# Performance work log

Hardware: AMD Instinct MI355X
Metric: run time of the kernel (lower is better)

## Reference

```python
import jax, jax.numpy as jnp
import numpy as np

DIM = 1024
HEADS = 16
HEAD_DIM = DIM // HEADS
SCALE = HEAD_DIM ** -0.5


def setup_inputs() -> dict:
    key = jax.random.key(0)
    k_x, k_wqkv, k_bqkv, k_wp, k_bp = jax.random.split(key, 5)
    B, N, C = 8, 1024, DIM
    lim_qkv = 1.0 / np.sqrt(C)
    x = jax.random.normal(k_x, (B, N, C), dtype=jnp.float32)
    # store weights in [in, out] layout (torch Linear weight is [out,in]; y = x @ W.T + b)
    W_qkv = jax.random.uniform(k_wqkv, (C, 3 * C), dtype=jnp.float32, minval=-lim_qkv, maxval=lim_qkv)
    b_qkv = jax.random.uniform(k_bqkv, (3 * C,), dtype=jnp.float32, minval=-lim_qkv, maxval=lim_qkv)
    W_proj = jax.random.uniform(k_wp, (C, C), dtype=jnp.float32, minval=-lim_qkv, maxval=lim_qkv)
    b_proj = jax.random.uniform(k_bp, (C,), dtype=jnp.float32, minval=-lim_qkv, maxval=lim_qkv)
    return {"x": x, "W_qkv": W_qkv, "b_qkv": b_qkv, "W_proj": W_proj, "b_proj": b_proj}


def reference(x, W_qkv, b_qkv, W_proj, b_proj):
    B, N, C = x.shape
    H, D = HEADS, C // HEADS
    qkv = x @ W_qkv + b_qkv                          # [B, N, 3C]
    qkv = qkv.reshape(B, N, 3, H, D)
    q, k, v = jnp.moveaxis(qkv, 2, 0)                # each [B, N, H, D]
    q = q.transpose(0, 2, 1, 3)                      # [B, H, N, D]
    k = k.transpose(0, 2, 1, 3)
    v = v.transpose(0, 2, 1, 3)
    attn = jnp.einsum("bhnd,bhmd->bhnm", q, k) * SCALE
    attn = jax.nn.softmax(attn, axis=-1)
    out = jnp.einsum("bhnm,bhmd->bhnd", attn, v)     # [B, H, N, D]
    out = out.transpose(0, 2, 1, 3).reshape(B, N, C)
    return out @ W_proj + b_proj
```

## Files before the change

### kernel.cpp

```cpp
#include <hip/hip_runtime.h>
#include <hip/hip_bf16.h>


using bf16x8 = __attribute__((ext_vector_type(8))) short;
using f32x4  = __attribute__((ext_vector_type(4))) float;
using u16    = unsigned short;
using u16x4  = __attribute__((ext_vector_type(4))) unsigned short;
using u16x8  = __attribute__((ext_vector_type(8))) unsigned short;
using u32x2  = __attribute__((ext_vector_type(2))) unsigned int;

__device__ __forceinline__ u16 f2bf(float f) {
  unsigned int u = __float_as_uint(f);
  u += 0x7FFFu + ((u >> 16) & 1u);
  return (u16)(u >> 16);
}
__device__ __forceinline__ float bf2f(u16 h) {
  return __uint_as_float(((unsigned int)h) << 16);
}
__device__ __forceinline__ unsigned cvt_pk_bf16(float a, float b) {
  unsigned r;
  asm("v_cvt_pk_bf16_f32 %0, %1, %2" : "=v"(r) : "v"(a), "v"(b));
  return r;
}
__device__ __forceinline__ float fexp2(float x) {
#if __has_builtin(__builtin_amdgcn_exp2f)
  return __builtin_amdgcn_exp2f(x);
#else
  return exp2f(x);
#endif
}

__device__ __forceinline__ void gload16(const u16* g, u16* lbase, int lane) {
#if __has_builtin(__builtin_amdgcn_global_load_lds)
  __builtin_amdgcn_global_load_lds(
      (const __attribute__((address_space(1))) void*)g,
      (__attribute__((address_space(3))) void*)lbase, 16, 0, 0);
#else
  *(u16x8*)(lbase + (size_t)lane * 8) = *(const u16x8*)g;
#endif
}

__global__ __launch_bounds__(256) void convert_f32_bf16(
    const float* __restrict__ in, u16* __restrict__ out)
{
  size_t i = ((size_t)blockIdx.x * 256 + threadIdx.x) * 8;
  f32x4 a = *(const f32x4*)(in + i);
  f32x4 b = *(const f32x4*)(in + i + 4);
  u16x8 h = { f2bf(a.x), f2bf(a.y), f2bf(a.z), f2bf(a.w),
              f2bf(b.x), f2bf(b.y), f2bf(b.z), f2bf(b.w) };
  *(u16x8*)(out + i) = h;
}

__global__ __launch_bounds__(256) void transpose_w(
    const float* __restrict__ W, u16* __restrict__ Wt, int K, int N)
{
  __shared__ float T[64][65];
  const int t = threadIdx.x;
  const int n0 = blockIdx.x * 64, k0 = blockIdx.y * 64;
  const int r = t >> 4, c4 = (t & 15) * 4;
  #pragma unroll
  for (int i = 0; i < 4; ++i) {
    f32x4 v = *(const f32x4*)&W[(size_t)(k0 + r + i * 16) * N + n0 + c4];
    T[r + i * 16][c4 + 0] = v.x;
    T[r + i * 16][c4 + 1] = v.y;
    T[r + i * 16][c4 + 2] = v.z;
    T[r + i * 16][c4 + 3] = v.w;
  }
  __syncthreads();
  const int nr = t >> 2, cs = (t & 3) * 16;
  u16x8 h0, h1;
  #pragma unroll
  for (int j = 0; j < 8; ++j) h0[j] = f2bf(T[cs + j][nr]);
  #pragma unroll
  for (int j = 0; j < 8; ++j) h1[j] = f2bf(T[cs + 8 + j][nr]);
  u16* dst = Wt + (size_t)(n0 + nr) * K + k0 + cs;
  *(u16x8*)dst = h0;
  *(u16x8*)(dst + 8) = h1;
}

__global__ __launch_bounds__(256) void v_transpose(
    const u16* __restrict__ Vr, u16* __restrict__ Vt)
{
  __shared__ u16 T[64 * 70];
  const int bh = blockIdx.x >> 4, nc = blockIdx.x & 15;
  const int t = threadIdx.x;
  const int r = t >> 2, c = (t & 3) * 16;
  const u16* src = Vr + ((size_t)bh * 1024 + nc * 64 + r) * 64 + c;
  *(u16x8*)&T[r * 70 + c]     = *(const u16x8*)src;
  *(u16x8*)&T[r * 70 + c + 8] = *(const u16x8*)(src + 8);
  __syncthreads();
  const int d = t >> 2, n0 = (t & 3) * 16;
  u16x8 o0, o1;
  #pragma unroll
  for (int j = 0; j < 8; ++j) o0[j] = T[(n0 + j) * 70 + d];
  #pragma unroll
  for (int j = 0; j < 8; ++j) o1[j] = T[(n0 + 8 + j) * 70 + d];
  u16* dst = Vt + ((size_t)bh * 64 + d) * 1024 + nc * 64 + n0;
  *(u16x8*)dst = o0;
  *(u16x8*)(dst + 8) = o1;
}

__global__ __launch_bounds__(256, 2) void qkv_gemm2(
    const u16* __restrict__ Xb, const u16* __restrict__ Wt,
    const float* __restrict__ bias,
    u16* __restrict__ Qb, u16* __restrict__ Kb, u16* __restrict__ Vr)
{
  constexpr int KD = 1024;
  __shared__ __align__(16) u16 As[128 * 32];
  __shared__ __align__(16) u16 Bs[128 * 32];

  const int tid = threadIdx.x;
  const int lane = tid & 63, wid = tid >> 6;
  const int wr = wid >> 1, wc = wid & 1;
  const int lg = lane >> 4, lc = lane & 15;
  const int row0 = blockIdx.x * 128, col0 = blockIdx.y * 128;

  f32x4 acc[4][4];
  #pragma unroll
  for (int m = 0; m < 4; ++m)
    #pragma unroll
    for (int n = 0; n < 4; ++n) acc[m][n] = (f32x4){0.f, 0.f, 0.f, 0.f};

  const int l4 = lane >> 2, ls = (lane & 3) * 8;
  const u16* gA0 = Xb + (size_t)(row0 + wid * 16 + l4) * KD + ls;
  const u16* gB0 = Wt + (size_t)(col0 + wid * 16 + l4) * KD + ls;
  u16* lA0 = As + wid * 512;
  u16* lB0 = Bs + wid * 512;

  for (int k0 = 0; k0 < KD; k0 += 32) {
    gload16(gA0 + k0, lA0, lane);
    gload16(gA0 + 64 * KD + k0, lA0 + 2048, lane);
    gload16(gB0 + k0, lB0, lane);
    gload16(gB0 + 64 * KD + k0, lB0 + 2048, lane);
    __syncthreads();

    bf16x8 a[4], b[4];
    #pragma unroll
    for (int m = 0; m < 4; ++m)
      a[m] = *(const bf16x8*)(As + (wr * 64 + m * 16 + lc) * 32 + lg * 8);
    #pragma unroll
    for (int n = 0; n < 4; ++n)
      b[n] = *(const bf16x8*)(Bs + (wc * 64 + n * 16 + lc) * 32 + lg * 8);
    #pragma unroll
    for (int m = 0; m < 4; ++m)
      #pragma unroll
      for (int n = 0; n < 4; ++n)
        acc[m][n] = __builtin_amdgcn_mfma_f32_16x16x32_bf16(a[m], b[n], acc[m][n], 0, 0, 0);
    __syncthreads();
  }

  #pragma unroll
  for (int m = 0; m < 4; ++m) {
    #pragma unroll
    for (int n = 0; n < 4; ++n) {
      const int gcb = col0 + wc * 64 + n * 16;
      const int which = gcb >> 10;
      const int gc = gcb + lc;
      const float bv = bias[gc];
      const int ci = gc & 1023, h = ci >> 6, d = ci & 63;
      const int gr0 = row0 + wr * 64 + m * 16 + lg * 4;
      const int bb = gr0 >> 10, nn0 = gr0 & 1023;
      u16* dst = (which == 0) ? Qb : (which == 1) ? Kb : Vr;
      #pragma unroll
      for (int r = 0; r < 4; ++r)
        dst[((size_t)(bb * 16 + h) * 1024 + nn0 + r) * 64 + d] =
            f2bf(acc[m][n][r] + bv);
    }
  }
}

__global__ __launch_bounds__(256, 2) void attn_kernel(
    const u16* __restrict__ Q, const u16* __restrict__ K,
    const u16* __restrict__ Vt, u16* __restrict__ O)
{
  __shared__ __align__(16) u16 Ks[64 * 64];
  __shared__ __align__(16) u16 Vs[64 * 64];
  __shared__ __align__(16) u16 Pl[4 * 32 * 72];

  const int tid = threadIdx.x, lane = tid & 63, wid = tid >> 6;
  const int lg = lane >> 4, lc = lane & 15;
  const int bh = blockIdx.x;
  const int qt = blockIdx.y;
  const size_t base = (size_t)bh * 65536;
  const u16* Qp = Q + base;
  const u16* Kp = K + base;
  const u16* Vp = Vt + base;

  const float QSCALE = 0.125f * 1.44269504f;
  bf16x8 qf[2][2];
  #pragma unroll
  for (int f = 0; f < 2; ++f) {
    const u16* qsrc = Qp + (size_t)(qt * 128 + wid * 32 + f * 16 + lc) * 64 + lg * 8;
    #pragma unroll
    for (int ks = 0; ks < 2; ++ks) {
      u16x8 raw = *(const u16x8*)(qsrc + ks * 32);
      bf16x8 t;
      #pragma unroll
      for (int j = 0; j < 8; ++j) t[j] = (short)f2bf(bf2f(raw[j]) * QSCALE);
      qf[f][ks] = t;
    }
  }

  f32x4 o[2][4];
  #pragma unroll
  for (int f = 0; f < 2; ++f)
    #pragma unroll
    for (int d = 0; d < 4; ++d) o[f][d] = (f32x4){0.f, 0.f, 0.f, 0.f};
  float m_r[2] = {-1e30f, -1e30f};
  float l_r[2] = {0.f, 0.f};

  const int srow  = lane >> 3;
  const int sslot = (lane & 7) ^ srow;
  const u16* gK0 = Kp + (size_t)(wid * 16 + srow) * 64 + sslot * 8;
  const u16* gV0 = Vp + (size_t)(wid * 16 + srow) * 1024 + sslot * 8;
  u16* lK0 = Ks + wid * 1024;
  u16* lV0 = Vs + wid * 1024;

  const int xr = lc & 7;
  const int cof0 = ((0 + lg) ^ xr) * 8;
  const int cof1 = ((4 + lg) ^ xr) * 8;
  const int prow = (wid * 32 + lc) * 72;

  for (int kt = 0; kt < 16; ++kt) {
    gload16(gK0 + kt * 4096, lK0, lane);
    gload16(gK0 + kt * 4096 + 512, lK0 + 512, lane);
    gload16(gV0 + kt * 64, lV0, lane);
    gload16(gV0 + 8192 + kt * 64, lV0 + 512, lane);
    __syncthreads();

    f32x4 s[2][4];
    #pragma unroll
    for (int f = 0; f < 2; ++f)
      #pragma unroll
      for (int kb = 0; kb < 4; ++kb) s[f][kb] = (f32x4){0.f, 0.f, 0.f, 0.f};
    #pragma unroll
    for (int ks = 0; ks < 2; ++ks) {
      const int co = ks ? cof1 : cof0;
      #pragma unroll
      for (int kb = 0; kb < 4; ++kb) {
        bf16x8 kfr = *(const bf16x8*)(Ks + (kb * 16 + lc) * 64 + co);
        s[0][kb] = __builtin_amdgcn_mfma_f32_16x16x32_bf16(kfr, qf[0][ks], s[0][kb], 0, 0, 0);
        s[1][kb] = __builtin_amdgcn_mfma_f32_16x16x32_bf16(kfr, qf[1][ks], s[1][kb], 0, 0, 0);
      }
    }

    #pragma unroll
    for (int f = 0; f < 2; ++f) {
      f32x4 t01, t23;
      #pragma unroll
      for (int c = 0; c < 4; ++c) {
        t01[c] = fmaxf(s[f][0][c], s[f][1][c]);
        t23[c] = fmaxf(s[f][2][c], s[f][3][c]);
      }
      float t = fmaxf(fmaxf(fmaxf(t01[0], t01[1]), fmaxf(t01[2], t01[3])),
                      fmaxf(fmaxf(t23[0], t23[1]), fmaxf(t23[2], t23[3])));
      t = fmaxf(t, __shfl_xor(t, 16));
      t = fmaxf(t, __shfl_xor(t, 32));

      if (!__all((t - m_r[f]) <= 11.5f)) {
        float nm = fmaxf(m_r[f], t);
        float sc = fexp2(m_r[f] - nm);
        m_r[f] = nm;
        l_r[f] *= sc;
        #pragma unroll
        for (int r = 0; r < 4; ++r) {
          float scr = __shfl(sc, lg * 4 + r, 16);
          #pragma unroll
          for (int d = 0; d < 4; ++d) o[f][d][r] *= scr;
        }
      }

      float lsum = 0.f;
      #pragma unroll
      for (int kb = 0; kb < 4; ++kb) {
        f32x4 p;
        #pragma unroll
        for (int c = 0; c < 4; ++c) {
          p[c] = fexp2(s[f][kb][c] - m_r[f]);
          lsum += p[c];
        }
        u32x2 w = { cvt_pk_bf16(p[0], p[1]), cvt_pk_bf16(p[2], p[3]) };
        *(u32x2*)(Pl + prow + f * 1152 + kb * 16 + lg * 4) = w;
      }
      l_r[f] += lsum;
    }

    bf16x8 pa[2][2];
    #pragma unroll
    for (int f = 0; f < 2; ++f)
      #pragma unroll
      for (int ks = 0; ks < 2; ++ks)
        pa[f][ks] = *(const bf16x8*)(Pl + prow + f * 1152 + ks * 32 + lg * 8);
    #pragma unroll
    for (int d = 0; d < 4; ++d) {
      #pragma unroll
      for (int ks = 0; ks < 2; ++ks) {
        const int co = ks ? cof1 : cof0;
        bf16x8 vfr = *(const bf16x8*)(Vs + (d * 16 + lc) * 64 + co);
        o[0][d] = __builtin_amdgcn_mfma_f32_16x16x32_bf16(pa[0][ks], vfr, o[0][d], 0, 0, 0);
        o[1][d] = __builtin_amdgcn_mfma_f32_16x16x32_bf16(pa[1][ks], vfr, o[1][d], 0, 0, 0);
      }
    }
    __syncthreads();
  }

  const int b = bh >> 4, h = bh & 15;
  #pragma unroll
  for (int f = 0; f < 2; ++f) {
    float t = l_r[f];
    t += __shfl_xor(t, 16);
    t += __shfl_xor(t, 32);
    float linv = 1.0f / t;
    #pragma unroll
    for (int r = 0; r < 4; ++r) {
      float li = __shfl(linv, lg * 4 + r, 16);
      int n = qt * 128 + wid * 32 + f * 16 + lg * 4 + r;
      u16* dst = O + ((size_t)b * 1024 + n) * 1024 + h * 64 + lc;
      #pragma unroll
      for (int d = 0; d < 4; ++d) dst[d * 16] = f2bf(o[f][d][r] * li);
    }
  }
}

__global__ __launch_bounds__(256, 2) void proj_gemm2(
    const u16* __restrict__ Ab, const u16* __restrict__ Wt,
    const float* __restrict__ bias, float* __restrict__ Out)
{
  constexpr int KD = 1024, NCOL = 1024;
  __shared__ __align__(16) u16 As[128 * 32];
  __shared__ __align__(16) u16 Bs[128 * 32];

  const int tid = threadIdx.x;
  const int lane = tid & 63, wid = tid >> 6;
  const int wr = wid >> 1, wc = wid & 1;
  const int lg = lane >> 4, lc = lane & 15;
  const int row0 = blockIdx.x * 128, col0 = blockIdx.y * 128;

  f32x4 acc[4][4];
  #pragma unroll
  for (int m = 0; m < 4; ++m)
    #pragma unroll
    for (int n = 0; n < 4; ++n) acc[m][n] = (f32x4){0.f, 0.f, 0.f, 0.f};

  const int l4 = lane >> 2, ls = (lane & 3) * 8;
  const u16* gA0 = Ab + (size_t)(row0 + wid * 16 + l4) * KD + ls;
  const u16* gB0 = Wt + (size_t)(col0 + wid * 16 + l4) * KD + ls;
  u16* lA0 = As + wid * 512;
  u16* lB0 = Bs + wid * 512;

  for (int k0 = 0; k0 < KD; k0 += 32) {
    gload16(gA0 + k0, lA0, lane);
    gload16(gA0 + 64 * KD + k0, lA0 + 2048, lane);
    gload16(gB0 + k0, lB0, lane);
    gload16(gB0 + 64 * KD + k0, lB0 + 2048, lane);
    __syncthreads();

    bf16x8 a[4], b[4];
    #pragma unroll
    for (int m = 0; m < 4; ++m)
      a[m] = *(const bf16x8*)(As + (wr * 64 + m * 16 + lc) * 32 + lg * 8);
    #pragma unroll
    for (int n = 0; n < 4; ++n)
      b[n] = *(const bf16x8*)(Bs + (wc * 64 + n * 16 + lc) * 32 + lg * 8);
    #pragma unroll
    for (int m = 0; m < 4; ++m)
      #pragma unroll
      for (int n = 0; n < 4; ++n)
        acc[m][n] = __builtin_amdgcn_mfma_f32_16x16x32_bf16(a[m], b[n], acc[m][n], 0, 0, 0);
    __syncthreads();
  }

  #pragma unroll
  for (int m = 0; m < 4; ++m) {
    #pragma unroll
    for (int n = 0; n < 4; ++n) {
      #pragma unroll
      for (int r = 0; r < 4; ++r) {
        int gr = row0 + wr * 64 + m * 16 + lg * 4 + r;
        int gc = col0 + wc * 64 + n * 16 + lc;
        Out[(size_t)gr * NCOL + gc] = acc[m][n][r] + bias[gc];
      }
    }
  }
}

extern "C" void kernel_launch(void* const* d_in, const int* in_sizes, int n_in,
                              void* d_out, int out_size, void* d_ws, size_t ws_size,
                              hipStream_t stream) {
  const float* x     = (const float*)d_in[0];
  const float* W_qkv = (const float*)d_in[1];
  const float* b_qkv = (const float*)d_in[2];
  const float* W_prj = (const float*)d_in[3];
  const float* b_prj = (const float*)d_in[4];
  float* out = (float*)d_out;

  const size_t SEG = (size_t)8192 * 1024;
  char* ws = (char*)d_ws;
  u16* Xb  = (u16*)ws;
  u16* Ab  = Xb;
  u16* VtG = (u16*)(ws + SEG * 2);
  u16* Wqt = (u16*)(ws + SEG * 4);
  u16* Wpt = Wqt + (size_t)3072 * 1024;
  u16* Vr  = (u16*)(ws + 41943040);
  u16* Qb  = (u16*)d_out;
  u16* Kb  = Qb + SEG;

  convert_f32_bf16<<<4096, 256, 0, stream>>>(x, Xb);
  transpose_w<<<dim3(48, 16), 256, 0, stream>>>(W_qkv, Wqt, 1024, 3072);
  transpose_w<<<dim3(16, 16), 256, 0, stream>>>(W_prj, Wpt, 1024, 1024);
  qkv_gemm2<<<dim3(64, 24), 256, 0, stream>>>(Xb, Wqt, b_qkv, Qb, Kb, Vr);
  v_transpose<<<2048, 256, 0, stream>>>(Vr, VtG);
  attn_kernel<<<dim3(128, 8), 256, 0, stream>>>(Qb, Kb, VtG, Ab);
  proj_gemm2<<<dim3(64, 8), 256, 0, stream>>>(Ab, Wpt, b_prj, out);
}
```

Measured before the change: 167.1 us.

## Rewrite QKV and proj GEMMs with double-buffered 128x256 tiles and swizzled LDS

Replaces the two 128x128 GEMM kernels with a shared 512-thread main loop that computes 128x256 tiles and uses K-steps of 64. Global-to-LDS loads are double-buffered with explicit vmcnt waits and raw barriers, so the next stage loads while MFMAs run on the current one. An XOR swizzle on the LDS layout is meant to avoid bank conflicts, and s_setprio raises priority around the MFMA bursts. The cost is more LDS per block (96KB), one block per CU, and fewer blocks in the grid, which can reduce latency hiding.

```diff
diff --git a/kernel.cpp b/kernel.cpp
--- a/kernel.cpp
+++ b/kernel.cpp
@@ -100,71 +100,116 @@
   *(u16x8*)(dst + 8) = o1;
 }
 
-__global__ __launch_bounds__(256, 2) void qkv_gemm2(
+#define GEMM_MAIN_LOOP(ABASE, BBASE)                                          \
+  const int tid = threadIdx.x;                                                \
+  const int lane = tid & 63, wid = tid >> 6;                                  \
+  const int wr = wid >> 2, wc = wid & 3;                                      \
+  const int lg = lane >> 4, lc = lane & 15;                                   \
+  const int row0 = blockIdx.x * 128, col0 = blockIdx.y * 256;                 \
+  f32x4 acc[4][4];                                                            \
+  _Pragma("unroll")                                                           \
+  for (int m = 0; m < 4; ++m)                                                 \
+    _Pragma("unroll")                                                         \
+    for (int n = 0; n < 4; ++n) acc[m][n] = (f32x4){0.f, 0.f, 0.f, 0.f};      \
+     \
+  const int swz = ((tid & 7) ^ ((tid >> 3) & 7)) * 8;                         \
+  const u16* gA0 = (ABASE) + (size_t)(row0 + (tid >> 3)) * 1024 + swz;        \
+  const u16* gA1 = (ABASE) + (size_t)(row0 + 64 + (tid >> 3)) * 1024 + swz;   \
+  const u16* gB0 = (BBASE) + (size_t)(col0 + (tid >> 3)) * 1024 + swz;        \
+  const u16* gB1 = (BBASE) + (size_t)(col0 + 64 + (tid >> 3)) * 1024 + swz;   \
+  const u16* gB2 = (BBASE) + (size_t)(col0 + 128 + (tid >> 3)) * 1024 + swz;  \
+  const u16* gB3 = (BBASE) + (size_t)(col0 + 192 + (tid >> 3)) * 1024 + swz;  \
+  u16* lA = LA + wid * 512;                                                   \
+  u16* lB = LB + wid * 512;                                                   \
+  auto STAGE = [&](int tt) {                                                  \
+    const int bA = (tt & 1) * 8192, bB = (tt & 1) * 16384, ko = tt * 64;      \
+    gload16(gA0 + ko, lA + bA, lane);                                         \
+    gload16(gA1 + ko, lA + bA + 4096, lane);                                  \
+    gload16(gB0 + ko, lB + bB, lane);                                         \
+    gload16(gB1 + ko, lB + bB + 4096, lane);                                  \
+    gload16(gB2 + ko, lB + bB + 8192, lane);                                  \
+    gload16(gB3 + ko, lB + bB + 12288, lane);                                 \
+  };                                                                          \
+  STAGE(0);                                                                   \
+  STAGE(1);                                                                   \
+                               \
+  const int xr = lc & 7;                                                      \
+  const int sl0 = (lg ^ xr) * 8, sl1 = ((4 + lg) ^ xr) * 8;                   \
+  const int arow = (wr * 64 + lc) * 64, brow = (wc * 64 + lc) * 64;           \
+  for (int t = 0; t < 16; ++t) {                                              \
+    if (t < 15) asm volatile("s_waitcnt vmcnt(6)" ::: "memory");              \
+    else        asm volatile("s_waitcnt vmcnt(0)" ::: "memory");              \
+    __builtin_amdgcn_s_barrier();                                             \
+    const int bA = (t & 1) * 8192, bB = (t & 1) * 16384;                      \
+    _Pragma("unroll")                                                         \
+    for (int ks = 0; ks < 2; ++ks) {                                          \
+      const int sl = ks ? sl1 : sl0;                                          \
+      bf16x8 a[4], b[4];                                                      \
+      _Pragma("unroll")                                                       \
+      for (int m = 0; m < 4; ++m)                                             \
+        a[m] = *(const bf16x8*)(LA + bA + arow + m * 1024 + sl);              \
+      _Pragma("unroll")                                                       \
+      for (int n = 0; n < 4; ++n)                                             \
+        b[n] = *(const bf16x8*)(LB + bB + brow + n * 1024 + sl);              \
+      __builtin_amdgcn_s_setprio(1);                                          \
+      _Pragma("unroll")                                                       \
+      for (int m = 0; m < 4; ++m)                                             \
+        _Pragma("unroll")                                                     \
+        for (int n = 0; n < 4; ++n)                                           \
+          acc[m][n] = __builtin_amdgcn_mfma_f32_16x16x32_bf16(                \
+              a[m], b[n], acc[m][n], 0, 0, 0);                                \
+      __builtin_amdgcn_s_setprio(0);                                          \
+    }                                                                         \
+    __builtin_amdgcn_s_barrier();                                             \
+    if (t + 2 < 16) STAGE(t + 2);                                             \
+  }
+
+__global__ __launch_bounds__(512, 1) void qkv_gemm3(
     const u16* __restrict__ Xb, const u16* __restrict__ Wt,
     const float* __restrict__ bias,
     u16* __restrict__ Qb, u16* __restrict__ Kb, u16* __restrict__ Vr)
 {
-  constexpr int KD = 1024;
-  __shared__ __align__(16) u16 As[128 * 32];
-  __shared__ __align__(16) u16 Bs[128 * 32];
-
-  const int tid = threadIdx.x;
-  const int lane = tid & 63, wid = tid >> 6;
-  const int wr = wid >> 1, wc = wid & 1;
-  const int lg = lane >> 4, lc = lane & 15;
-  const int row0 = blockIdx.x * 128, col0 = blockIdx.y * 128;
-
-  f32x4 acc[4][4];
-  #pragma unroll
-  for (int m = 0; m < 4; ++m)
-    #pragma unroll
-    for (int n = 0; n < 4; ++n) acc[m][n] = (f32x4){0.f, 0.f, 0.f, 0.f};
-
-  const int l4 = lane >> 2, ls = (lane & 3) * 8;
-  const u16* gA0 = Xb + (size_t)(row0 + wid * 16 + l4) * KD + ls;
-  const u16* gB0 = Wt + (size_t)(col0 + wid * 16 + l4) * KD + ls;
-  u16* lA0 = As + wid * 512;
-  u16* lB0 = Bs + wid * 512;
-
-  for (int k0 = 0; k0 < KD; k0 += 32) {
-    gload16(gA0 + k0, lA0, lane);
-    gload16(gA0 + 64 * KD + k0, lA0 + 2048, lane);
-    gload16(gB0 + k0, lB0, lane);
-    gload16(gB0 + 64 * KD + k0, lB0 + 2048, lane);
-    __syncthreads();
-
-    bf16x8 a[4], b[4];
-    #pragma unroll
-    for (int m = 0; m < 4; ++m)
-      a[m] = *(const bf16x8*)(As + (wr * 64 + m * 16 + lc) * 32 + lg * 8);
-    #pragma unroll
-    for (int n = 0; n < 4; ++n)
-      b[n] = *(const bf16x8*)(Bs + (wc * 64 + n * 16 + lc) * 32 + lg * 8);
-    #pragma unroll
-    for (int m = 0; m < 4; ++m)
-      #pragma unroll
-      for (int n = 0; n < 4; ++n)
-        acc[m][n] = __builtin_amdgcn_mfma_f32_16x16x32_bf16(a[m], b[n], acc[m][n], 0, 0, 0);
-    __syncthreads();
-  }
-
+  __shared__ __align__(16) u16 LA[2 * 128 * 64];
+  __shared__ __align__(16) u16 LB[2 * 256 * 64];
+  GEMM_MAIN_LOOP(Xb, Wt)
+
+  const int which = col0 >> 10;
+  u16* dst = (which == 0) ? Qb : (which == 1) ? Kb : Vr;
+  const int bb = row0 >> 10, nnb = (row0 & 1023) + wr * 64;
+  const int hb = ((col0 & 1023) >> 6) + wc;
   #pragma unroll
   for (int m = 0; m < 4; ++m) {
     #pragma unroll
     for (int n = 0; n < 4; ++n) {
-      const int gcb = col0 + wc * 64 + n * 16;
-      const int which = gcb >> 10;
-      const int gc = gcb + lc;
+      const int d = n * 16 + lc;
+      const float bv = bias[col0 + wc * 64 + n * 16 + lc];
+      const int nn0 = nnb + m * 16 + lg * 4;
+      #pragma unroll
+      for (int r = 0; r < 4; ++r)
+        dst[((size_t)(bb * 16 + hb) * 1024 + nn0 + r) * 64 + d] =
+            f2bf(acc[m][n][r] + bv);
+    }
+  }
+}
+
+__global__ __launch_bounds__(512, 1) void proj_gemm3(
+    const u16* __restrict__ Ab, const u16* __restrict__ Wt,
+    const float* __restrict__ bias, float* __restrict__ Out)
+{
+  __shared__ __align__(16) u16 LA[2 * 128 * 64];
+  __shared__ __align__(16) u16 LB[2 * 256 * 64];
+  GEMM_MAIN_LOOP(Ab, Wt)
+
+  #pragma unroll
+  for (int m = 0; m < 4; ++m) {
+    #pragma unroll
+    for (int n = 0; n < 4; ++n) {
+      const int gc = col0 + wc * 64 + n * 16 + lc;
       const float bv = bias[gc];
-      const int ci = gc & 1023, h = ci >> 6, d = ci & 63;
       const int gr0 = row0 + wr * 64 + m * 16 + lg * 4;
-      const int bb = gr0 >> 10, nn0 = gr0 & 1023;
-      u16* dst = (which == 0) ? Qb : (which == 1) ? Kb : Vr;
       #pragma unroll
       for (int r = 0; r < 4; ++r)
-        dst[((size_t)(bb * 16 + h) * 1024 + nn0 + r) * 64 + d] =
-            f2bf(acc[m][n][r] + bv);
+        Out[(size_t)(gr0 + r) * 1024 + gc] = acc[m][n][r] + bv;
     }
   }
 }
@@ -322,68 +367,6 @@
   }
 }
 
-__global__ __launch_bounds__(256, 2) void proj_gemm2(
-    const u16* __restrict__ Ab, const u16* __restrict__ Wt,
-    const float* __restrict__ bias, float* __restrict__ Out)
-{
-  constexpr int KD = 1024, NCOL = 1024;
-  __shared__ __align__(16) u16 As[128 * 32];
-  __shared__ __align__(16) u16 Bs[128 * 32];
-
-  const int tid = threadIdx.x;
-  const int lane = tid & 63, wid = tid >> 6;
-  const int wr = wid >> 1, wc = wid & 1;
-  const int lg = lane >> 4, lc = lane & 15;
-  const int row0 = blockIdx.x * 128, col0 = blockIdx.y * 128;
-
-  f32x4 acc[4][4];
-  #pragma unroll
-  for (int m = 0; m < 4; ++m)
-    #pragma unroll
-    for (int n = 0; n < 4; ++n) acc[m][n] = (f32x4){0.f, 0.f, 0.f, 0.f};
-
-  const int l4 = lane >> 2, ls = (lane & 3) * 8;
-  const u16* gA0 = Ab + (size_t)(row0 + wid * 16 + l4) * KD + ls;
-  const u16* gB0 = Wt + (size_t)(col0 + wid * 16 + l4) * KD + ls;
-  u16* lA0 = As + wid * 512;
-  u16* lB0 = Bs + wid * 512;
-
-  for (int k0 = 0; k0 < KD; k0 += 32) {
-    gload16(gA0 + k0, lA0, lane);
-    gload16(gA0 + 64 * KD + k0, lA0 + 2048, lane);
-    gload16(gB0 + k0, lB0, lane);
-    gload16(gB0 + 64 * KD + k0, lB0 + 2048, lane);
-    __syncthreads();
-
-    bf16x8 a[4], b[4];
-    #pragma unroll
-    for (int m = 0; m < 4; ++m)
-      a[m] = *(const bf16x8*)(As + (wr * 64 + m * 16 + lc) * 32 + lg * 8);
-    #pragma unroll
-    for (int n = 0; n < 4; ++n)
-      b[n] = *(const bf16x8*)(Bs + (wc * 64 + n * 16 + lc) * 32 + lg * 8);
-    #pragma unroll
-    for (int m = 0; m < 4; ++m)
-      #pragma unroll
-      for (int n = 0; n < 4; ++n)
-        acc[m][n] = __builtin_amdgcn_mfma_f32_16x16x32_bf16(a[m], b[n], acc[m][n], 0, 0, 0);
-    __syncthreads();
-  }
-
-  #pragma unroll
-  for (int m = 0; m < 4; ++m) {
-    #pragma unroll
-    for (int n = 0; n < 4; ++n) {
-      #pragma unroll
-      for (int r = 0; r < 4; ++r) {
-        int gr = row0 + wr * 64 + m * 16 + lg * 4 + r;
-        int gc = col0 + wc * 64 + n * 16 + lc;
-        Out[(size_t)gr * NCOL + gc] = acc[m][n][r] + bias[gc];
-      }
-    }
-  }
-}
-
 extern "C" void kernel_launch(void* const* d_in, const int* in_sizes, int n_in,
                               void* d_out, int out_size, void* d_ws, size_t ws_size,
                               hipStream_t stream) {
@@ -408,8 +391,8 @@
   convert_f32_bf16<<<4096, 256, 0, stream>>>(x, Xb);
   transpose_w<<<dim3(48, 16), 256, 0, stream>>>(W_qkv, Wqt, 1024, 3072);
   transpose_w<<<dim3(16, 16), 256, 0, stream>>>(W_prj, Wpt, 1024, 1024);
-  qkv_gemm2<<<dim3(64, 24), 256, 0, stream>>>(Xb, Wqt, b_qkv, Qb, Kb, Vr);
+  qkv_gemm3<<<dim3(64, 12), 512, 0, stream>>>(Xb, Wqt, b_qkv, Qb, Kb, Vr);
   v_transpose<<<2048, 256, 0, stream>>>(Vr, VtG);
   attn_kernel<<<dim3(128, 8), 256, 0, stream>>>(Qb, Kb, VtG, Ab);
-  proj_gemm2<<<dim3(64, 8), 256, 0, stream>>>(Ab, Wpt, b_prj, out);
-}
+  proj_gemm3<<<dim3(64, 4), 512, 0, stream>>>(Ab, Wpt, b_prj, out);
+}
```

New measurement: 171.2 us. 1.02x slower.

## Rewrite QKV GEMM with 256x256 tiles, double-buffered swizzled LDS and staged prefetch

Applied to the files above, without the earlier changes.

Replaces the 128x128, single-buffered QKV GEMM with a 512-thread 256x256 tile kernel that uses K-step 64, double-buffered LDS with XOR swizzle to avoid bank conflicts, and interleaves global prefetch of the next tile with MFMA phases under explicit waitcnt and barriers. Raising setprio around MFMA blocks aims to keep the matrix cores busy. The larger tile raises data reuse per load, but it drops to one block per CU and uses 128 KB of LDS, and only 384 blocks are launched.

```diff
diff --git a/kernel.cpp b/kernel.cpp
--- a/kernel.cpp
+++ b/kernel.cpp
@@ -100,71 +100,126 @@
   *(u16x8*)(dst + 8) = o1;
 }
 
-__global__ __launch_bounds__(256, 2) void qkv_gemm2(
+__global__ __launch_bounds__(512, 1) void qkv_gemm4(
     const u16* __restrict__ Xb, const u16* __restrict__ Wt,
     const float* __restrict__ bias,
     u16* __restrict__ Qb, u16* __restrict__ Kb, u16* __restrict__ Vr)
 {
-  constexpr int KD = 1024;
-  __shared__ __align__(16) u16 As[128 * 32];
-  __shared__ __align__(16) u16 Bs[128 * 32];
+  __shared__ __align__(16) u16 LA[2 * 256 * 64];
+  __shared__ __align__(16) u16 LB[2 * 256 * 64];
 
   const int tid = threadIdx.x;
   const int lane = tid & 63, wid = tid >> 6;
-  const int wr = wid >> 1, wc = wid & 1;
+  const int wm = wid >> 2, wn = wid & 3;
   const int lg = lane >> 4, lc = lane & 15;
-  const int row0 = blockIdx.x * 128, col0 = blockIdx.y * 128;
-
-  f32x4 acc[4][4];
-  #pragma unroll
-  for (int m = 0; m < 4; ++m)
+  const int row0 = blockIdx.x * 256, col0 = blockIdx.y * 256;
+
+  f32x4 acc[8][4];
+  #pragma unroll
+  for (int m = 0; m < 8; ++m)
     #pragma unroll
     for (int n = 0; n < 4; ++n) acc[m][n] = (f32x4){0.f, 0.f, 0.f, 0.f};
 
-  const int l4 = lane >> 2, ls = (lane & 3) * 8;
-  const u16* gA0 = Xb + (size_t)(row0 + wid * 16 + l4) * KD + ls;
-  const u16* gB0 = Wt + (size_t)(col0 + wid * 16 + l4) * KD + ls;
-  u16* lA0 = As + wid * 512;
-  u16* lB0 = Bs + wid * 512;
-
-  for (int k0 = 0; k0 < KD; k0 += 32) {
-    gload16(gA0 + k0, lA0, lane);
-    gload16(gA0 + 64 * KD + k0, lA0 + 2048, lane);
-    gload16(gB0 + k0, lB0, lane);
-    gload16(gB0 + 64 * KD + k0, lB0 + 2048, lane);
-    __syncthreads();
-
-    bf16x8 a[4], b[4];
-    #pragma unroll
-    for (int m = 0; m < 4; ++m)
-      a[m] = *(const bf16x8*)(As + (wr * 64 + m * 16 + lc) * 32 + lg * 8);
-    #pragma unroll
-    for (int n = 0; n < 4; ++n)
-      b[n] = *(const bf16x8*)(Bs + (wc * 64 + n * 16 + lc) * 32 + lg * 8);
-    #pragma unroll
-    for (int m = 0; m < 4; ++m)
-      #pragma unroll
-      for (int n = 0; n < 4; ++n)
-        acc[m][n] = __builtin_amdgcn_mfma_f32_16x16x32_bf16(a[m], b[n], acc[m][n], 0, 0, 0);
-    __syncthreads();
-  }
-
-  #pragma unroll
-  for (int m = 0; m < 4; ++m) {
-    #pragma unroll
-    for (int n = 0; n < 4; ++n) {
-      const int gcb = col0 + wc * 64 + n * 16;
-      const int which = gcb >> 10;
-      const int gc = gcb + lc;
-      const float bv = bias[gc];
-      const int ci = gc & 1023, h = ci >> 6, d = ci & 63;
-      const int gr0 = row0 + wr * 64 + m * 16 + lg * 4;
-      const int bb = gr0 >> 10, nn0 = gr0 & 1023;
-      u16* dst = (which == 0) ? Qb : (which == 1) ? Kb : Vr;
+  const int srow = tid >> 3;
+  const int swz = ((tid & 7) ^ ((tid >> 3) & 7)) * 8;
+  const u16* gA = Xb + (size_t)(row0 + srow) * 1024 + swz;
+  const u16* gB = Wt + (size_t)(col0 + srow) * 1024 + swz;
+  u16* lAw = LA + wid * 512;
+  u16* lBw = LB + wid * 512;
+
+  #define STAGE_A(tt, R0) gload16(gA + (size_t)(R0) * 1024 + (tt) * 64, \
+                                  lAw + ((tt) & 1) * 16384 + (R0) * 64, lane)
+  #define STAGE_B(tt, R0) gload16(gB + (size_t)(R0) * 1024 + (tt) * 64, \
+                                  lBw + ((tt) & 1) * 16384 + (R0) * 64, lane)
+
+  STAGE_A(0, 0); STAGE_A(0, 64); STAGE_A(0, 128); STAGE_A(0, 192);
+  STAGE_B(0, 0); STAGE_B(0, 64); STAGE_B(0, 128); STAGE_B(0, 192);
+
+  const int xr = lc & 7;
+  const int sl0 = (lg ^ xr) * 8, sl1 = ((4 + lg) ^ xr) * 8;
+  const int abase = (wm * 128 + lc) * 64;
+  const int bbase = (wn * 64 + lc) * 64;
+
+  bf16x8 b[4][2];
+
+  for (int t = 0; t < 16; ++t) {
+    const int cb = (t & 1) * 16384;
+
+    if (t + 1 < 16) { STAGE_A(t + 1, 0); STAGE_A(t + 1, 64); }
+    if (t + 1 < 16) asm volatile("s_waitcnt vmcnt(2)" ::: "memory");
+    else            asm volatile("s_waitcnt vmcnt(0)" ::: "memory");
+    __builtin_amdgcn_s_barrier();
+
+    bf16x8 a2[2][2];
+    #pragma unroll
+    for (int fn = 0; fn < 4; ++fn) {
+      b[fn][0] = *(const bf16x8*)(LB + cb + bbase + fn * 1024 + sl0);
+      b[fn][1] = *(const bf16x8*)(LB + cb + bbase + fn * 1024 + sl1);
+    }
+    #pragma unroll
+    for (int i = 0; i < 2; ++i) {
+      a2[i][0] = *(const bf16x8*)(LA + cb + abase + i * 1024 + sl0);
+      a2[i][1] = *(const bf16x8*)(LA + cb + abase + i * 1024 + sl1);
+    }
+    asm volatile("s_waitcnt lgkmcnt(0)" ::: "memory");
+    __builtin_amdgcn_sched_barrier(0);
+    __builtin_amdgcn_s_setprio(1);
+    #pragma unroll
+    for (int i = 0; i < 2; ++i)
+      #pragma unroll
+      for (int fn = 0; fn < 4; ++fn) {
+        acc[i][fn] = __builtin_amdgcn_mfma_f32_16x16x32_bf16(a2[i][0], b[fn][0], acc[i][fn], 0, 0, 0);
+        acc[i][fn] = __builtin_amdgcn_mfma_f32_16x16x32_bf16(a2[i][1], b[fn][1], acc[i][fn], 0, 0, 0);
+      }
+    __builtin_amdgcn_s_setprio(0);
+    __builtin_amdgcn_s_barrier();
+
+    #pragma unroll
+    for (int p = 1; p < 4; ++p) {
+      bf16x8 ap[2][2];
+      #pragma unroll
+      for (int i = 0; i < 2; ++i) {
+        ap[i][0] = *(const bf16x8*)(LA + cb + abase + (2 * p + i) * 1024 + sl0);
+        ap[i][1] = *(const bf16x8*)(LA + cb + abase + (2 * p + i) * 1024 + sl1);
+      }
+      if (t + 1 < 16) {
+        if (p == 1)      { STAGE_A(t + 1, 128); STAGE_A(t + 1, 192); }
+        else if (p == 2) { STAGE_B(t + 1, 0);   STAGE_B(t + 1, 64);  }
+        else             { STAGE_B(t + 1, 128); STAGE_B(t + 1, 192); }
+      }
+      __builtin_amdgcn_s_barrier();
+      asm volatile("s_waitcnt lgkmcnt(0)" ::: "memory");
+      __builtin_amdgcn_sched_barrier(0);
+      __builtin_amdgcn_s_setprio(1);
+      #pragma unroll
+      for (int i = 0; i < 2; ++i)
+        #pragma unroll
+        for (int fn = 0; fn < 4; ++fn) {
+          acc[2 * p + i][fn] = __builtin_amdgcn_mfma_f32_16x16x32_bf16(ap[i][0], b[fn][0], acc[2 * p + i][fn], 0, 0, 0);
+          acc[2 * p + i][fn] = __builtin_amdgcn_mfma_f32_16x16x32_bf16(ap[i][1], b[fn][1], acc[2 * p + i][fn], 0, 0, 0);
+        }
+      __builtin_amdgcn_s_setprio(0);
+      __builtin_amdgcn_s_barrier();
+    }
+  }
+  #undef STAGE_A
+  #undef STAGE_B
+
+  const int which = col0 >> 10;
+  u16* dst = (which == 0) ? Qb : (which == 1) ? Kb : Vr;
+  const int bb = row0 >> 10;
+  const int hb = ((col0 & 1023) >> 6) + wn;
+  #pragma unroll
+  for (int fm = 0; fm < 8; ++fm) {
+    const int nn0 = (row0 & 1023) + wm * 128 + fm * 16 + lg * 4;
+    #pragma unroll
+    for (int fn = 0; fn < 4; ++fn) {
+      const int d = fn * 16 + lc;
+      const float bv = bias[col0 + wn * 64 + fn * 16 + lc];
       #pragma unroll
       for (int r = 0; r < 4; ++r)
-        dst[((size_t)(bb * 16 + h) * 1024 + nn0 + r) * 64 + d] =
-            f2bf(acc[m][n][r] + bv);
+        dst[((size_t)(bb * 16 + hb) * 1024 + nn0 + r) * 64 + d] =
+            f2bf(acc[fm][fn][r] + bv);
     }
   }
 }
@@ -408,7 +463,7 @@
   convert_f32_bf16<<<4096, 256, 0, stream>>>(x, Xb);
   transpose_w<<<dim3(48, 16), 256, 0, stream>>>(W_qkv, Wqt, 1024, 3072);
   transpose_w<<<dim3(16, 16), 256, 0, stream>>>(W_prj, Wpt, 1024, 1024);
-  qkv_gemm2<<<dim3(64, 24), 256, 0, stream>>>(Xb, Wqt, b_qkv, Qb, Kb, Vr);
+  qkv_gemm4<<<dim3(32, 12), 512, 0, stream>>>(Xb, Wqt, b_qkv, Qb, Kb, Vr);
   v_transpose<<<2048, 256, 0, stream>>>(Vr, VtG);
   attn_kernel<<<dim3(128, 8), 256, 0, stream>>>(Qb, Kb, VtG, Ab);
   proj_gemm2<<<dim3(64, 8), 256, 0, stream>>>(Ab, Wpt, b_prj, out);
```

Measured after the change: 178.2 us. +6.6%, slower.

## Merge prep kernels into one launch and fuse V transpose into QKV GEMM epilogue

Applied to the files above, without the earlier changes.

Combines the x conversion and the two weight transposes into a single prep kernel that dispatches on block index. The QKV GEMM epilogue for V tiles now stages the output in shared memory and writes V directly in transposed layout, which removes the separate v_transpose kernel and its round trip through global memory. Shared memory per GEMM block grows to about 33KB, which could affect occupancy at two blocks per CU.

```diff
diff --git a/kernel.cpp b/kernel.cpp
--- a/kernel.cpp
+++ b/kernel.cpp
@@ -5,7 +5,6 @@
 using bf16x8 = __attribute__((ext_vector_type(8))) short;
 using f32x4  = __attribute__((ext_vector_type(4))) float;
 using u16    = unsigned short;
-using u16x4  = __attribute__((ext_vector_type(4))) unsigned short;
 using u16x8  = __attribute__((ext_vector_type(8))) unsigned short;
 using u32x2  = __attribute__((ext_vector_type(2))) unsigned int;
 
@@ -40,23 +39,10 @@
 #endif
 }
 
-__global__ __launch_bounds__(256) void convert_f32_bf16(
-    const float* __restrict__ in, u16* __restrict__ out)
+__device__ __forceinline__ void transpose_tile(
+    const float* __restrict__ W, u16* __restrict__ Wt, int K, int N,
+    int n0, int k0, float (*T)[65], int t)
 {
-  size_t i = ((size_t)blockIdx.x * 256 + threadIdx.x) * 8;
-  f32x4 a = *(const f32x4*)(in + i);
-  f32x4 b = *(const f32x4*)(in + i + 4);
-  u16x8 h = { f2bf(a.x), f2bf(a.y), f2bf(a.z), f2bf(a.w),
-              f2bf(b.x), f2bf(b.y), f2bf(b.z), f2bf(b.w) };
-  *(u16x8*)(out + i) = h;
-}
-
-__global__ __launch_bounds__(256) void transpose_w(
-    const float* __restrict__ W, u16* __restrict__ Wt, int K, int N)
-{
-  __shared__ float T[64][65];
-  const int t = threadIdx.x;
-  const int n0 = blockIdx.x * 64, k0 = blockIdx.y * 64;
   const int r = t >> 4, c4 = (t & 15) * 4;
   #pragma unroll
   for (int i = 0; i < 4; ++i) {
@@ -78,36 +64,39 @@
   *(u16x8*)(dst + 8) = h1;
 }
 
-__global__ __launch_bounds__(256) void v_transpose(
-    const u16* __restrict__ Vr, u16* __restrict__ Vt)
+__global__ __launch_bounds__(256) void prep(
+    const float* __restrict__ x, u16* __restrict__ Xb,
+    const float* __restrict__ Wq, u16* __restrict__ Wqt,
+    const float* __restrict__ Wp, u16* __restrict__ Wpt)
 {
-  __shared__ u16 T[64 * 70];
-  const int bh = blockIdx.x >> 4, nc = blockIdx.x & 15;
-  const int t = threadIdx.x;
-  const int r = t >> 2, c = (t & 3) * 16;
-  const u16* src = Vr + ((size_t)bh * 1024 + nc * 64 + r) * 64 + c;
-  *(u16x8*)&T[r * 70 + c]     = *(const u16x8*)src;
-  *(u16x8*)&T[r * 70 + c + 8] = *(const u16x8*)(src + 8);
-  __syncthreads();
-  const int d = t >> 2, n0 = (t & 3) * 16;
-  u16x8 o0, o1;
-  #pragma unroll
-  for (int j = 0; j < 8; ++j) o0[j] = T[(n0 + j) * 70 + d];
-  #pragma unroll
-  for (int j = 0; j < 8; ++j) o1[j] = T[(n0 + 8 + j) * 70 + d];
-  u16* dst = Vt + ((size_t)bh * 64 + d) * 1024 + nc * 64 + n0;
-  *(u16x8*)dst = o0;
-  *(u16x8*)(dst + 8) = o1;
+  __shared__ float T[64][65];
+  const int bid = blockIdx.x, t = threadIdx.x;
+  if (bid < 4096) {
+    size_t i = ((size_t)bid * 256 + t) * 8;
+    f32x4 a = *(const f32x4*)(x + i);
+    f32x4 b = *(const f32x4*)(x + i + 4);
+    u16x8 h = { f2bf(a.x), f2bf(a.y), f2bf(a.z), f2bf(a.w),
+                f2bf(b.x), f2bf(b.y), f2bf(b.z), f2bf(b.w) };
+    *(u16x8*)(Xb + i) = h;
+  } else if (bid < 4864) {
+    const int tb = bid - 4096;
+    transpose_tile(Wq, Wqt, 1024, 3072, (tb % 48) * 64, (tb / 48) * 64, T, t);
+  } else {
+    const int tb = bid - 4864;
+    transpose_tile(Wp, Wpt, 1024, 1024, (tb % 16) * 64, (tb / 16) * 64, T, t);
+  }
 }
 
 __global__ __launch_bounds__(256, 2) void qkv_gemm2(
     const u16* __restrict__ Xb, const u16* __restrict__ Wt,
     const float* __restrict__ bias,
-    u16* __restrict__ Qb, u16* __restrict__ Kb, u16* __restrict__ Vr)
+    u16* __restrict__ Qb, u16* __restrict__ Kb, u16* __restrict__ VtG)
 {
   constexpr int KD = 1024;
-  __shared__ __align__(16) u16 As[128 * 32];
-  __shared__ __align__(16) u16 Bs[128 * 32];
+  __shared__ __align__(16) u16 SM[128 * 130];
+  u16* As = SM;
+  u16* Bs = SM + 4096;
+  u16* Tv = SM;
 
   const int tid = threadIdx.x;
   const int lane = tid & 63, wid = tid >> 6;
@@ -149,22 +138,51 @@
     __syncthreads();
   }
 
-  #pragma unroll
-  for (int m = 0; m < 4; ++m) {
-    #pragma unroll
-    for (int n = 0; n < 4; ++n) {
-      const int gcb = col0 + wc * 64 + n * 16;
-      const int which = gcb >> 10;
-      const int gc = gcb + lc;
-      const float bv = bias[gc];
-      const int ci = gc & 1023, h = ci >> 6, d = ci & 63;
-      const int gr0 = row0 + wr * 64 + m * 16 + lg * 4;
-      const int bb = gr0 >> 10, nn0 = gr0 & 1023;
-      u16* dst = (which == 0) ? Qb : (which == 1) ? Kb : Vr;
-      #pragma unroll
-      for (int r = 0; r < 4; ++r)
-        dst[((size_t)(bb * 16 + h) * 1024 + nn0 + r) * 64 + d] =
-            f2bf(acc[m][n][r] + bv);
+  const int which = col0 >> 10;
+  if (which == 2) {
+    #pragma unroll
+    for (int m = 0; m < 4; ++m) {
+      #pragma unroll
+      for (int n = 0; n < 4; ++n) {
+        const int col = wc * 64 + n * 16 + lc;
+        const float bv = bias[col0 + col];
+        const int rrow = wr * 64 + m * 16 + lg * 4;
+        #pragma unroll
+        for (int r = 0; r < 4; ++r)
+          Tv[(rrow + r) * 130 + col] = f2bf(acc[m][n][r] + bv);
+      }
+    }
+    __syncthreads();
+    const int c = tid >> 1, half = tid & 1;
+    const int hh = c >> 6, d = c & 63;
+    const int bb = row0 >> 10, nb = row0 & 1023;
+    const int hbase = (col0 & 1023) >> 6;
+    u16* vdst = VtG + ((size_t)(bb * 16 + hbase + hh) * 64 + d) * 1024
+                + nb + half * 64;
+    #pragma unroll
+    for (int g = 0; g < 8; ++g) {
+      u16x8 o;
+      #pragma unroll
+      for (int j = 0; j < 8; ++j)
+        o[j] = Tv[(half * 64 + g * 8 + j) * 130 + c];
+      *(u16x8*)(vdst + g * 8) = o;
+    }
+  } else {
+    u16* dst = (which == 0) ? Qb : Kb;
+    #pragma unroll
+    for (int m = 0; m < 4; ++m) {
+      #pragma unroll
+      for (int n = 0; n < 4; ++n) {
+        const int gc = col0 + wc * 64 + n * 16 + lc;
+        const float bv = bias[gc];
+        const int ci = gc & 1023, h = ci >> 6, d = ci & 63;
+        const int gr0 = row0 + wr * 64 + m * 16 + lg * 4;
+        const int bb = gr0 >> 10, nn0 = gr0 & 1023;
+        #pragma unroll
+        for (int r = 0; r < 4; ++r)
+          dst[((size_t)(bb * 16 + h) * 1024 + nn0 + r) * 64 + d] =
+              f2bf(acc[m][n][r] + bv);
+      }
     }
   }
 }
@@ -401,15 +419,11 @@
   u16* VtG = (u16*)(ws + SEG * 2);
   u16* Wqt = (u16*)(ws + SEG * 4);
   u16* Wpt = Wqt + (size_t)3072 * 1024;
-  u16* Vr  = (u16*)(ws + 41943040);
   u16* Qb  = (u16*)d_out;
   u16* Kb  = Qb + SEG;
 
-  convert_f32_bf16<<<4096, 256, 0, stream>>>(x, Xb);
-  transpose_w<<<dim3(48, 16), 256, 0, stream>>>(W_qkv, Wqt, 1024, 3072);
-  transpose_w<<<dim3(16, 16), 256, 0, stream>>>(W_prj, Wpt, 1024, 1024);
-  qkv_gemm2<<<dim3(64, 24), 256, 0, stream>>>(Xb, Wqt, b_qkv, Qb, Kb, Vr);
-  v_transpose<<<2048, 256, 0, stream>>>(Vr, VtG);
+  prep<<<5120, 256, 0, stream>>>(x, Xb, W_qkv, Wqt, W_prj, Wpt);
+  qkv_gemm2<<<dim3(64, 24), 256, 0, stream>>>(Xb, Wqt, b_qkv, Qb, Kb, VtG);
   attn_kernel<<<dim3(128, 8), 256, 0, stream>>>(Qb, Kb, VtG, Ab);
   proj_gemm2<<<dim3(64, 8), 256, 0, stream>>>(Ab, Wpt, b_prj, out);
 }
```

Measured after the change: 159.7 us. 1.05x faster.
